# Optimization experiments

Hardware: AMD Instinct MI355X
Metric: run time of the kernel (lower is better)

## Reference

```python
import jax, jax.numpy as jnp
import numpy as np

NEG_SLOPE = 0.2  # PyG GATConv default leaky_relu slope
N_NODES, IN_DIM, HID, HEADS, OUT = 50000, 128, 64, 4, 128
N_EDGES = 800000


def gat_conv(x, src, dst, num_nodes, W, a_src, a_dst, bias, concat):
    """One PyG-style GATConv (add_self_loops already applied to src/dst)."""
    H, C = a_src.shape
    xp = (x @ W).reshape(num_nodes, H, C)            # (N,H,C)
    s = jnp.einsum('nhc,hc->nh', xp, a_src)          # per-node src score
    d = jnp.einsum('nhc,hc->nh', xp, a_dst)          # per-node dst score
    e = s[src] + d[dst]                              # (E,H)
    e = jnp.where(e > 0, e, NEG_SLOPE * e)           # leaky_relu
    # segment softmax over edges grouped by destination node
    m = jax.ops.segment_max(e, dst, num_segments=num_nodes)
    p = jnp.exp(e - m[dst])
    z = jax.ops.segment_sum(p, dst, num_segments=num_nodes)
    alpha = p / (z[dst] + 1e-16)                     # (E,H)
    # scatter-aggregate messages
    out = jax.ops.segment_sum(xp[src] * alpha[:, :, None], dst, num_segments=num_nodes)
    out = out.reshape(num_nodes, H * C) if concat else out.mean(axis=1)
    return out + bias


def setup_inputs() -> dict:
    key = jax.random.key(0)
    ks = jax.random.split(key, 16)
    HC = HEADS * HID
    inp = {
        'x': jax.random.normal(ks[0], (N_NODES, IN_DIM), dtype=jnp.float32),
        'edge_index': jax.random.randint(ks[1], (2, N_EDGES), 0, N_NODES, dtype=jnp.int32),
        'W0': jax.random.normal(ks[2], (IN_DIM, HC), dtype=jnp.float32) * 0.08,
        'a_src0': jax.random.normal(ks[3], (HEADS, HID), dtype=jnp.float32) * 0.1,
        'a_dst0': jax.random.normal(ks[4], (HEADS, HID), dtype=jnp.float32) * 0.1,
        'b0': jnp.zeros((HC,), dtype=jnp.float32),
        'W1': jax.random.normal(ks[5], (HC, HC), dtype=jnp.float32) * 0.06,
        'a_src1': jax.random.normal(ks[6], (HEADS, HID), dtype=jnp.float32) * 0.1,
        'a_dst1': jax.random.normal(ks[7], (HEADS, HID), dtype=jnp.float32) * 0.1,
        'b1': jnp.zeros((HC,), dtype=jnp.float32),
        'W2': jax.random.normal(ks[8], (HC, OUT), dtype=jnp.float32) * 0.06,
        'a_src2': jax.random.normal(ks[9], (1, OUT), dtype=jnp.float32) * 0.1,
        'a_dst2': jax.random.normal(ks[10], (1, OUT), dtype=jnp.float32) * 0.1,
        'b2': jnp.zeros((OUT,), dtype=jnp.float32),
    }
    return inp


def reference(x, edge_index, W0, a_src0, a_dst0, b0, W1, a_src1, a_dst1, b1, W2, a_src2, a_dst2, b2):
    N = x.shape[0]
    loops = jnp.arange(N, dtype=edge_index.dtype)  # add_self_loops=True
    src = jnp.concatenate([edge_index[0], loops])
    dst = jnp.concatenate([edge_index[1], loops])
    h = gat_conv(x, src, dst, N, W0, a_src0, a_dst0, b0, True)
    h = jax.nn.elu(h)
    h = gat_conv(h, src, dst, N, W1, a_src1, a_dst1, b1, True)
    h = jax.nn.elu(h)
    h = gat_conv(h, src, dst, N, W2, a_src2, a_dst2, b2, False)
    return h
```

## Files before the change

### kernel.cpp

```cpp
#include <hip/hip_runtime.h>
#include <hip/hip_bf16.h>
#include <hip/hip_fp16.h>
#include <math.h>

#define N_NODES 50000
#define N_EDGES 800000
#define ET      (N_EDGES + N_NODES)
#define IN_DIM  128
#define HEADS   4
#define HID     64
#define HC      256
#define OUTD    128

typedef _Float16 half8 __attribute__((ext_vector_type(8)));
typedef float f32x4 __attribute__((ext_vector_type(4)));


__global__ void hist_k(const int* __restrict__ ei, int* __restrict__ counts) {
    int i = blockIdx.x * blockDim.x + threadIdx.x;
    if (i >= ET) return;
    int dv = (i < N_EDGES) ? ei[N_EDGES + i] : (i - N_EDGES);
    atomicAdd(&counts[dv], 1);
}

__global__ void scan1_k(const int* __restrict__ counts, int* __restrict__ offs,
                        int* __restrict__ bsums) {
    __shared__ int sm[512];
    int tid = threadIdx.x;
    int i = blockIdx.x * 512 + tid;
    int v = (i < N_NODES) ? counts[i] : 0;
    sm[tid] = v;
    __syncthreads();
    #pragma unroll
    for (int o = 1; o < 512; o <<= 1) {
        int add = (tid >= o) ? sm[tid - o] : 0;
        __syncthreads();
        sm[tid] += add;
        __syncthreads();
    }
    if (i < N_NODES) offs[i] = sm[tid] - v;
    if (tid == 511) bsums[blockIdx.x] = sm[511];
}

__global__ void scan2_k(int* __restrict__ bsums, int nb) {
    __shared__ int sm[128];
    int tid = threadIdx.x;
    int v = (tid < nb) ? bsums[tid] : 0;
    sm[tid] = v;
    __syncthreads();
    #pragma unroll
    for (int o = 1; o < 128; o <<= 1) {
        int add = (tid >= o) ? sm[tid - o] : 0;
        __syncthreads();
        sm[tid] += add;
        __syncthreads();
    }
    if (tid < nb) bsums[tid] = sm[tid] - v;
}

__global__ void scan3_k(int* __restrict__ offs, const int* __restrict__ bsums) {
    int i = blockIdx.x * 512 + threadIdx.x;
    if (i < N_NODES) offs[i] += bsums[blockIdx.x];
    if (i == 0) offs[N_NODES] = ET;
}

__global__ void fill_k(const int* __restrict__ ei, const int* __restrict__ offs,
                       int* __restrict__ cursor, int* __restrict__ csr) {
    int i = blockIdx.x * blockDim.x + threadIdx.x;
    if (i >= ET) return;
    int sv, dv;
    if (i < N_EDGES) { sv = ei[i]; dv = ei[N_EDGES + i]; }
    else             { sv = dv = i - N_EDGES; }
    int pos = offs[dv] + atomicAdd(&cursor[dv], 1);
    csr[pos] = sv;
}


__global__ void cvt_fp16_k(const float* __restrict__ x, __half* __restrict__ xh, int n4) {
    int i = blockIdx.x * 256 + threadIdx.x;
    if (i >= n4) return;
    float4 v = *(const float4*)(x + (size_t)i * 4);
    union { __half2 h2[2]; float2 f2; } u;
    u.h2[0] = __floats2half2_rn(v.x, v.y);
    u.h2[1] = __floats2half2_rn(v.z, v.w);
    *(float2*)(xh + (size_t)i * 4) = u.f2;
}

__global__ void wtrans_k(const float* __restrict__ W, __half* __restrict__ Wt, int K, int N) {
    int idx = blockIdx.x * 256 + threadIdx.x;
    if (idx >= K * N) return;
    int n = idx / K, k = idx - n * K;
    Wt[idx] = __float2half(W[(size_t)k * N + n]);
}


__device__ __forceinline__ void async_copy16(void* lds_base, const void* gaddr) {
    __builtin_amdgcn_global_load_lds(
        (const __attribute__((address_space(1))) unsigned int*)gaddr,
        (__attribute__((address_space(3))) unsigned int*)lds_base,
        16, 0, 0);
}

__global__ __launch_bounds__(256) void gemm_mfma_k(const __half* __restrict__ A,
                                                   const __half* __restrict__ Wt,
                                                   __half* __restrict__ C,
                                                   int M, int K, int N) {
    __shared__ __attribute__((aligned(16))) __half Ah[128 * 32];
    __shared__ __attribute__((aligned(16))) __half Bh[128 * 32];
    const int t = threadIdx.x;
    const int w = t >> 6;
    const int lane = t & 63;
    const int wm = w >> 1, wn = w & 1;
    const int row0 = blockIdx.x * 128;
    const int col0 = blockIdx.y * 128;

    f32x4 acc[4][4];
    #pragma unroll
    for (int i = 0; i < 4; ++i)
        #pragma unroll
        for (int j = 0; j < 4; ++j) acc[i][j] = (f32x4){0.f, 0.f, 0.f, 0.f};

    const int srow = lane >> 2;
    const int skq  = (lane & 3) * 8;
    const int fr = lane & 15;
    const int fq = (lane >> 4) * 8;

    for (int k0 = 0; k0 < K; k0 += 32) {
        __syncthreads();
        #pragma unroll
        for (int hh = 0; hh < 2; ++hh) {
            int ra = row0 + w * 32 + hh * 16 + srow;
            if (ra > M - 1) ra = M - 1;
            async_copy16(&Ah[(w * 32 + hh * 16) * 32],
                         A + (size_t)ra * K + k0 + skq);
            int rb = col0 + w * 32 + hh * 16 + srow;
            async_copy16(&Bh[(w * 32 + hh * 16) * 32],
                         Wt + (size_t)rb * K + k0 + skq);
        }
        __syncthreads();
        half8 a[4], b[4];
        #pragma unroll
        for (int i = 0; i < 4; ++i)
            a[i] = *(const half8*)&Ah[(wm * 64 + i * 16 + fr) * 32 + fq];
        #pragma unroll
        for (int j = 0; j < 4; ++j)
            b[j] = *(const half8*)&Bh[(wn * 64 + j * 16 + fr) * 32 + fq];
        #pragma unroll
        for (int i = 0; i < 4; ++i)
            #pragma unroll
            for (int j = 0; j < 4; ++j)
                acc[i][j] = __builtin_amdgcn_mfma_f32_16x16x32_f16(a[i], b[j], acc[i][j], 0, 0, 0);
    }

    const int cr = (lane >> 4) * 4;
    const int cc = lane & 15;
    #pragma unroll
    for (int i = 0; i < 4; ++i) {
        #pragma unroll
        for (int j = 0; j < 4; ++j) {
            int c = col0 + wn * 64 + j * 16 + cc;
            #pragma unroll
            for (int reg = 0; reg < 4; ++reg) {
                int r = row0 + wm * 64 + i * 16 + cr + reg;
                if (r < M)
                    C[(size_t)r * N + c] = __float2half(acc[i][j][reg]);
            }
        }
    }
}


template<int H, int C>
__global__ __launch_bounds__(256) void scores_k(const __half* __restrict__ xp,
                                                const float* __restrict__ asrc,
                                                const float* __restrict__ adst,
                                                float* __restrict__ s,
                                                float* __restrict__ d) {
    constexpr int HCl = H * C;
    constexpr int EPL = HCl / 64;
    int wid = blockIdx.x * 4 + (threadIdx.x >> 6);
    int lane = threadIdx.x & 63;
    if (wid >= N_NODES) return;
    const __half* row = xp + (size_t)wid * HCl + lane * EPL;
    float v[EPL];
    if constexpr (EPL == 4) {
        union { float2 f2; __half2 h2[2]; } u;
        u.f2 = *(const float2*)row;
        float2 a = __half22float2(u.h2[0]);
        float2 b = __half22float2(u.h2[1]);
        v[0] = a.x; v[1] = a.y; v[2] = b.x; v[3] = b.y;
    } else {
        union { float f; __half2 h2; } u;
        u.f = *(const float*)row;
        float2 a = __half22float2(u.h2);
        v[0] = a.x; v[1] = a.y;
    }
    float ps = 0.f, pd = 0.f;
    #pragma unroll
    for (int k = 0; k < EPL; ++k) {
        ps += v[k] * asrc[lane * EPL + k];
        pd += v[k] * adst[lane * EPL + k];
    }
    constexpr int GW = 64 / H;
    #pragma unroll
    for (int o = 1; o < GW; o <<= 1) {
        ps += __shfl_xor(ps, o, 64);
        pd += __shfl_xor(pd, o, 64);
    }
    if ((lane & (GW - 1)) == 0) {
        int h = lane / GW;
        s[(size_t)wid * H + h] = ps;
        d[(size_t)wid * H + h] = pd;
    }
}


template<int H, int C, bool ELU_OUT, typename OT>
__global__ __launch_bounds__(256) void aggr_k(const __half* __restrict__ xp,
                                              const float* __restrict__ s,
                                              const float* __restrict__ d,
                                              const int* __restrict__ offs,
                                              const int* __restrict__ csr,
                                              const float* __restrict__ bias,
                                              OT* __restrict__ out) {
    constexpr int HCl = H * C;
    constexpr int EPL = HCl / 64;
    constexpr int U = 8;
    int wid = blockIdx.x * 4 + (threadIdx.x >> 6);
    int lane = threadIdx.x & 63;
    if (wid >= N_NODES) return;
    int h = (lane * EPL) / C;
    float dh = d[(size_t)wid * H + h];
    float z = 0.f;
    float acc[EPL];
    #pragma unroll
    for (int k = 0; k < EPL; ++k) acc[k] = 0.f;

    auto loadrow = [&](int src, float* v) {
        const __half* xr = xp + (size_t)src * HCl + lane * EPL;
        if constexpr (EPL == 4) {
            union { float2 f2; __half2 h2[2]; } u;
            u.f2 = *(const float2*)xr;
            float2 a = __half22float2(u.h2[0]);
            float2 b = __half22float2(u.h2[1]);
            v[0] = a.x; v[1] = a.y; v[2] = b.x; v[3] = b.y;
        } else {
            union { float f; __half2 h2; } u;
            u.f = *(const float*)xr;
            float2 a = __half22float2(u.h2);
            v[0] = a.x; v[1] = a.y;
        }
    };

    int e0 = offs[wid], e1 = offs[wid + 1];
    int j = e0;
    for (; j + U <= e1; j += U) {
        int srcs[U];
        #pragma unroll
        for (int u = 0; u < U; ++u) srcs[u] = csr[j + u];
        float ev[U];
        #pragma unroll
        for (int u = 0; u < U; ++u) ev[u] = s[(size_t)srcs[u] * H + h];
        float v[U][EPL];
        #pragma unroll
        for (int u = 0; u < U; ++u) loadrow(srcs[u], v[u]);
        #pragma unroll
        for (int u = 0; u < U; ++u) {
            float e = ev[u] + dh;
            e = (e > 0.f) ? e : 0.2f * e;
            float p = __expf(e);
            z += p;
            #pragma unroll
            for (int k = 0; k < EPL; ++k) acc[k] += p * v[u][k];
        }
    }
    for (; j < e1; ++j) {
        int sv = csr[j];
        float e = s[(size_t)sv * H + h] + dh;
        e = (e > 0.f) ? e : 0.2f * e;
        float p = __expf(e);
        float v[EPL];
        loadrow(sv, v);
        z += p;
        #pragma unroll
        for (int k = 0; k < EPL; ++k) acc[k] += p * v[k];
    }

    float inv = 1.f / (z + 1e-16f);
    float o[EPL];
    #pragma unroll
    for (int k = 0; k < EPL; ++k) {
        o[k] = acc[k] * inv + bias[lane * EPL + k];
        if constexpr (ELU_OUT) o[k] = (o[k] > 0.f) ? o[k] : (__expf(o[k]) - 1.f);
    }
    if constexpr (sizeof(OT) == 2 && EPL == 4) {
        union { __half2 h2[2]; float2 f2; } u;
        u.h2[0] = __floats2half2_rn(o[0], o[1]);
        u.h2[1] = __floats2half2_rn(o[2], o[3]);
        *(float2*)((__half*)out + (size_t)wid * HCl + lane * EPL) = u.f2;
    } else {
        #pragma unroll
        for (int k = 0; k < EPL; ++k)
            out[(size_t)wid * HCl + lane * EPL + k] = (OT)o[k];
    }
}


extern "C" void kernel_launch(void* const* d_in, const int* in_sizes, int n_in,
                              void* d_out, int out_size, void* d_ws, size_t ws_size,
                              hipStream_t stream) {
    const float* x      = (const float*)d_in[0];
    const int*   ei     = (const int*)  d_in[1];
    const float* W0     = (const float*)d_in[2];
    const float* as0    = (const float*)d_in[3];
    const float* ad0    = (const float*)d_in[4];
    const float* b0     = (const float*)d_in[5];
    const float* W1     = (const float*)d_in[6];
    const float* as1    = (const float*)d_in[7];
    const float* ad1    = (const float*)d_in[8];
    const float* b1     = (const float*)d_in[9];
    const float* W2     = (const float*)d_in[10];
    const float* as2    = (const float*)d_in[11];
    const float* ad2    = (const float*)d_in[12];
    const float* b2     = (const float*)d_in[13];
    float* out = (float*)d_out;

    char* p = (char*)d_ws;
    auto take = [&](size_t bytes) {
        char* r = p;
        p += (bytes + 255) & ~(size_t)255;
        return r;
    };
    __half* XPh   = (__half*)take((size_t)N_NODES * HC * 2);
    __half* Hbuf  = (__half*)take((size_t)N_NODES * HC * 2);
    __half* xh    = (__half*)take((size_t)N_NODES * IN_DIM * 2);
    __half* Wt0   = (__half*)take((size_t)IN_DIM * HC * 2);
    __half* Wt1   = (__half*)take((size_t)HC * HC * 2);
    __half* Wt2   = (__half*)take((size_t)HC * OUTD * 2);
    float*  S     = (float*) take((size_t)N_NODES * HEADS * 4);
    float*  D     = (float*) take((size_t)N_NODES * HEADS * 4);
    int*    counts= (int*)   take((size_t)2 * N_NODES * 4);
    int*    cursor= counts + N_NODES;
    int*    offs  = (int*)   take((size_t)(N_NODES + 1) * 4);
    int*    bsums = (int*)   take(512 * 4);
    int*    csr   = (int*)   take((size_t)ET * 4);

    const int NB_SCAN = (N_NODES + 511) / 512;
    const int ET_BLOCKS = (ET + 255) / 256;
    const int NODE_BLOCKS = (N_NODES + 3) / 4;

    hipMemsetAsync(counts, 0, (size_t)2 * N_NODES * 4, stream);
    hist_k<<<ET_BLOCKS, 256, 0, stream>>>(ei, counts);
    scan1_k<<<NB_SCAN, 512, 0, stream>>>(counts, offs, bsums);
    scan2_k<<<1, 128, 0, stream>>>(bsums, NB_SCAN);
    scan3_k<<<NB_SCAN, 512, 0, stream>>>(offs, bsums);
    fill_k<<<ET_BLOCKS, 256, 0, stream>>>(ei, offs, cursor, csr);

    cvt_fp16_k<<<(N_NODES * IN_DIM / 4 + 255) / 256, 256, 0, stream>>>(x, xh, N_NODES * IN_DIM / 4);
    wtrans_k<<<(IN_DIM * HC + 255) / 256, 256, 0, stream>>>(W0, Wt0, IN_DIM, HC);
    wtrans_k<<<(HC * HC + 255) / 256, 256, 0, stream>>>(W1, Wt1, HC, HC);
    wtrans_k<<<(HC * OUTD + 255) / 256, 256, 0, stream>>>(W2, Wt2, HC, OUTD);

    const int MB = (N_NODES + 127) / 128;
    dim3 g0(MB, HC / 128);
    dim3 g2(MB, OUTD / 128);

    gemm_mfma_k<<<g0, 256, 0, stream>>>(xh, Wt0, XPh, N_NODES, IN_DIM, HC);
    scores_k<HEADS, HID><<<NODE_BLOCKS, 256, 0, stream>>>(XPh, as0, ad0, S, D);
    aggr_k<HEADS, HID, true, __half><<<NODE_BLOCKS, 256, 0, stream>>>(XPh, S, D, offs, csr, b0, Hbuf);

    gemm_mfma_k<<<g0, 256, 0, stream>>>(Hbuf, Wt1, XPh, N_NODES, HC, HC);
    scores_k<HEADS, HID><<<NODE_BLOCKS, 256, 0, stream>>>(XPh, as1, ad1, S, D);
    aggr_k<HEADS, HID, true, __half><<<NODE_BLOCKS, 256, 0, stream>>>(XPh, S, D, offs, csr, b1, Hbuf);

    gemm_mfma_k<<<g2, 256, 0, stream>>>(Hbuf, Wt2, XPh, N_NODES, HC, OUTD);
    scores_k<1, OUTD><<<NODE_BLOCKS, 256, 0, stream>>>(XPh, as2, ad2, S, D);
    aggr_k<1, OUTD, false, float><<<NODE_BLOCKS, 256, 0, stream>>>(XPh, S, D, offs, csr, b2, out);
}
```

Measured before the change: 454.0 us.

## Fuse attention score computation into GEMM epilogue and sort CSR segments

Computes per-node source and destination attention scores directly from the GEMM accumulators in the epilogue, using a shuffle reduction. This removes the separate scores kernels that re-read the projected features. The single-head final layer uses atomics into zeroed buffers because one block holds all of its columns. It also adds a wave-level bitonic sort of each destination's source list, so gathers during aggregation walk memory in a more ordered way. The cost is extra epilogue work, extra register pressure and one added sort kernel.

```diff
diff --git a/kernel.cpp b/kernel.cpp
--- a/kernel.cpp
+++ b/kernel.cpp
@@ -75,6 +75,28 @@
     csr[pos] = sv;
 }
 
+__global__ __launch_bounds__(256) void sortseg_k(const int* __restrict__ offs,
+                                                 int* __restrict__ csr) {
+    int wid = blockIdx.x * 4 + (threadIdx.x >> 6);
+    int lane = threadIdx.x & 63;
+    if (wid >= N_NODES) return;
+    int e0 = offs[wid], e1 = offs[wid + 1];
+    int deg = e1 - e0;
+    if (deg <= 1 || deg > 64) return;
+    int v = (lane < deg) ? csr[e0 + lane] : 0x7fffffff;
+    #pragma unroll
+    for (int k = 2; k <= 64; k <<= 1) {
+        #pragma unroll
+        for (int j = k >> 1; j > 0; j >>= 1) {
+            int v2 = __shfl_xor(v, j, 64);
+            bool keepmin = (((lane & j) == 0) == ((lane & k) == 0));
+            int mn = min(v, v2), mx = max(v, v2);
+            v = keepmin ? mn : mx;
+        }
+    }
+    if (lane < deg) csr[e0 + lane] = v;
+}
+
 
 __global__ void cvt_fp16_k(const float* __restrict__ x, __half* __restrict__ xh, int n4) {
     int i = blockIdx.x * 256 + threadIdx.x;
@@ -101,9 +123,14 @@
         16, 0, 0);
 }
 
+template<int H, int CD, bool ATOMIC>
 __global__ __launch_bounds__(256) void gemm_mfma_k(const __half* __restrict__ A,
                                                    const __half* __restrict__ Wt,
                                                    __half* __restrict__ C,
+                                                   const float* __restrict__ asrc,
+                                                   const float* __restrict__ adst,
+                                                   float* __restrict__ S,
+                                                   float* __restrict__ D,
                                                    int M, int K, int N) {
     __shared__ __attribute__((aligned(16))) __half Ah[128 * 32];
     __shared__ __attribute__((aligned(16))) __half Bh[128 * 32];
@@ -167,50 +194,41 @@
             }
         }
     }
-}
-
-
-template<int H, int C>
-__global__ __launch_bounds__(256) void scores_k(const __half* __restrict__ xp,
-                                                const float* __restrict__ asrc,
-                                                const float* __restrict__ adst,
-                                                float* __restrict__ s,
-                                                float* __restrict__ d) {
-    constexpr int HCl = H * C;
-    constexpr int EPL = HCl / 64;
-    int wid = blockIdx.x * 4 + (threadIdx.x >> 6);
-    int lane = threadIdx.x & 63;
-    if (wid >= N_NODES) return;
-    const __half* row = xp + (size_t)wid * HCl + lane * EPL;
-    float v[EPL];
-    if constexpr (EPL == 4) {
-        union { float2 f2; __half2 h2[2]; } u;
-        u.f2 = *(const float2*)row;
-        float2 a = __half22float2(u.h2[0]);
-        float2 b = __half22float2(u.h2[1]);
-        v[0] = a.x; v[1] = a.y; v[2] = b.x; v[3] = b.y;
-    } else {
-        union { float f; __half2 h2; } u;
-        u.f = *(const float*)row;
-        float2 a = __half22float2(u.h2);
-        v[0] = a.x; v[1] = a.y;
-    }
-    float ps = 0.f, pd = 0.f;
-    #pragma unroll
-    for (int k = 0; k < EPL; ++k) {
-        ps += v[k] * asrc[lane * EPL + k];
-        pd += v[k] * adst[lane * EPL + k];
-    }
-    constexpr int GW = 64 / H;
-    #pragma unroll
-    for (int o = 1; o < GW; o <<= 1) {
-        ps += __shfl_xor(ps, o, 64);
-        pd += __shfl_xor(pd, o, 64);
-    }
-    if ((lane & (GW - 1)) == 0) {
-        int h = lane / GW;
-        s[(size_t)wid * H + h] = ps;
-        d[(size_t)wid * H + h] = pd;
+
+    const int hh_ = ATOMIC ? 0 : (blockIdx.y * 2 + wn);
+    float asj[4], adj[4];
+    #pragma unroll
+    for (int j = 0; j < 4; ++j) {
+        int cwh = (ATOMIC ? wn * 64 : 0) + j * 16 + cc;
+        asj[j] = asrc[hh_ * CD + cwh];
+        adj[j] = adst[hh_ * CD + cwh];
+    }
+    #pragma unroll
+    for (int i = 0; i < 4; ++i) {
+        #pragma unroll
+        for (int reg = 0; reg < 4; ++reg) {
+            float sv = 0.f, dv = 0.f;
+            #pragma unroll
+            for (int j = 0; j < 4; ++j) {
+                sv = fmaf(acc[i][j][reg], asj[j], sv);
+                dv = fmaf(acc[i][j][reg], adj[j], dv);
+            }
+            #pragma unroll
+            for (int o = 1; o < 16; o <<= 1) {
+                sv += __shfl_xor(sv, o, 64);
+                dv += __shfl_xor(dv, o, 64);
+            }
+            int r = row0 + wm * 64 + i * 16 + cr + reg;
+            if (cc == 0 && r < M) {
+                if constexpr (ATOMIC) {
+                    atomicAdd(&S[r], sv);
+                    atomicAdd(&D[r], dv);
+                } else {
+                    S[(size_t)r * H + hh_] = sv;
+                    D[(size_t)r * H + hh_] = dv;
+                }
+            }
+        }
     }
 }
 
@@ -355,6 +373,7 @@
     scan2_k<<<1, 128, 0, stream>>>(bsums, NB_SCAN);
     scan3_k<<<NB_SCAN, 512, 0, stream>>>(offs, bsums);
     fill_k<<<ET_BLOCKS, 256, 0, stream>>>(ei, offs, cursor, csr);
+    sortseg_k<<<NODE_BLOCKS, 256, 0, stream>>>(offs, csr);
 
     cvt_fp16_k<<<(N_NODES * IN_DIM / 4 + 255) / 256, 256, 0, stream>>>(x, xh, N_NODES * IN_DIM / 4);
     wtrans_k<<<(IN_DIM * HC + 255) / 256, 256, 0, stream>>>(W0, Wt0, IN_DIM, HC);
@@ -365,15 +384,14 @@
     dim3 g0(MB, HC / 128);
     dim3 g2(MB, OUTD / 128);
 
-    gemm_mfma_k<<<g0, 256, 0, stream>>>(xh, Wt0, XPh, N_NODES, IN_DIM, HC);
-    scores_k<HEADS, HID><<<NODE_BLOCKS, 256, 0, stream>>>(XPh, as0, ad0, S, D);
+    gemm_mfma_k<HEADS, HID, false><<<g0, 256, 0, stream>>>(xh, Wt0, XPh, as0, ad0, S, D, N_NODES, IN_DIM, HC);
     aggr_k<HEADS, HID, true, __half><<<NODE_BLOCKS, 256, 0, stream>>>(XPh, S, D, offs, csr, b0, Hbuf);
 
-    gemm_mfma_k<<<g0, 256, 0, stream>>>(Hbuf, Wt1, XPh, N_NODES, HC, HC);
-    scores_k<HEADS, HID><<<NODE_BLOCKS, 256, 0, stream>>>(XPh, as1, ad1, S, D);
+    gemm_mfma_k<HEADS, HID, false><<<g0, 256, 0, stream>>>(Hbuf, Wt1, XPh, as1, ad1, S, D, N_NODES, HC, HC);
     aggr_k<HEADS, HID, true, __half><<<NODE_BLOCKS, 256, 0, stream>>>(XPh, S, D, offs, csr, b1, Hbuf);
 
-    gemm_mfma_k<<<g2, 256, 0, stream>>>(Hbuf, Wt2, XPh, N_NODES, HC, OUTD);
-    scores_k<1, OUTD><<<NODE_BLOCKS, 256, 0, stream>>>(XPh, as2, ad2, S, D);
+    hipMemsetAsync(S, 0, (size_t)N_NODES * 4, stream);
+    hipMemsetAsync(D, 0, (size_t)N_NODES * 4, stream);
+    gemm_mfma_k<1, OUTD, true><<<g2, 256, 0, stream>>>(Hbuf, Wt2, XPh, as2, ad2, S, D, N_NODES, HC, OUTD);
     aggr_k<1, OUTD, false, float><<<NODE_BLOCKS, 256, 0, stream>>>(XPh, S, D, offs, csr, b2, out);
 }
```

Result: no change. 455.6 us (+0.4%).
